# Kernel tuning notes

Measured on AMD Instinct MI355X. Metric: run time of the kernel, lower is better.

The kernel has to match this reference:

```python
import jax, jax.numpy as jnp
import numpy as np
from jax import lax

# pywt db4 filters (8 taps)
_DEC_LO = np.array([-0.010597401784997278, 0.032883011666982945, 0.030841381835986965,
                    -0.18703481171888114, -0.02798376941698385, 0.6308807679295904,
                    0.7148465705525415, 0.23037781330885523])
_DEC_HI = np.array([-0.23037781330885523, 0.7148465705525415, -0.6308807679295904,
                    -0.02798376941698385, 0.18703481171888114, 0.030841381835986965,
                    -0.032883011666982945, -0.010597401784997278])
_REC_LO = _DEC_LO[::-1].copy()
_REC_HI = _DEC_HI[::-1].copy()
_L = 8  # filter length
LEVELS = 4


def _dwt_level(x):
    # x: (M, n) -> (cA, cD) each (M, (n+_L-1)//2), pywt 'symmetric' mode
    xe = jnp.pad(x, ((0, 0), (_L - 1, _L - 1)), mode='symmetric')[:, 1:]
    ker = jnp.stack([_DEC_LO[::-1], _DEC_HI[::-1]]).astype(x.dtype)[:, None, :]  # (2,1,L)
    y = lax.conv_general_dilated(xe[:, None, :], ker, (2,), 'VALID')  # (M,2,m)
    return y[:, 0], y[:, 1]


def _idwt_level(ca, cd, out_len):
    # inverse DWT, cropped to out_len (matches length of next-finer approximation)
    inp = jnp.stack([ca, cd], axis=1)  # (M,2,m)
    ker = jnp.stack([_REC_LO[::-1], _REC_HI[::-1]]).astype(ca.dtype)[None]  # (1,2,L)
    y = lax.conv_general_dilated(inp, ker, (1,), [(_L - 1, _L - 1)], lhs_dilation=(2,))
    return y[:, 0, _L - 2:_L - 2 + out_len]


def setup_inputs() -> dict:
    key = jax.random.key(0)
    k1, k2, k3, k4 = jax.random.split(key, 4)
    B, N, C = 32, 8192, 64
    m = N
    for _ in range(LEVELS):
        m = (m + _L - 1) // 2  # 518
    scale = 1.0 / (C * C)
    return {
        'x': jax.random.normal(k1, (B, N, C), jnp.float32),
        'w1': scale * jax.random.uniform(k2, (C, C, m), jnp.float32),
        'w2': scale * jax.random.uniform(k3, (C, C, m), jnp.float32),
        'dense_kernel': jax.random.normal(k4, (C, C), jnp.float32) / jnp.sqrt(C).astype(jnp.float32),
        'dense_bias': jnp.zeros((C,), jnp.float32),
    }


def reference(x, w1, w2, dense_kernel, dense_bias):
    B, N, C = x.shape
    xc = jnp.transpose(x, (0, 2, 1)).reshape(B * C, N)  # per-(batch,channel) signals
    # analysis: multi-level DWT
    lens, details = [], []
    a = xc
    for _ in range(LEVELS):
        lens.append(a.shape[1])
        a, d = _dwt_level(a)
        details.append(d)
    m = a.shape[1]
    # channel mixing on coarsest approximation and coarsest detail (WNO kernel)
    a = jnp.einsum('bim,iom->bom', a.reshape(B, C, m), w1).reshape(B * C, m)
    details[-1] = jnp.einsum('bim,iom->bom', details[-1].reshape(B, C, m), w2).reshape(B * C, m)
    # synthesis: multi-level IDWT
    for j in range(LEVELS - 1, -1, -1):
        a = _idwt_level(a, details[j], lens[j])
    y = jnp.transpose(a.reshape(B, C, N), (0, 2, 1))
    shortcut = x @ dense_kernel + dense_bias  # Dense 1x1 shortcut
    out = y + shortcut
    return out * jnp.tanh(jax.nn.softplus(out))  # mish
```

## Files before the change

### kernel.cpp

```cpp
#include <hip/hip_runtime.h>
#include <hip/hip_bf16.h>
#include <stdint.h>

typedef __attribute__((ext_vector_type(8))) short short8;
typedef __attribute__((ext_vector_type(4))) float floatx4;

__device__ __constant__ float c_DL[8] = {
    -0.010597401784997278f, 0.032883011666982945f, 0.030841381835986965f,
    -0.18703481171888114f, -0.02798376941698385f, 0.6308807679295904f,
    0.7148465705525415f, 0.23037781330885523f};
__device__ __constant__ float c_DH[8] = {
    -0.23037781330885523f, 0.7148465705525415f, -0.6308807679295904f,
    -0.02798376941698385f, 0.18703481171888114f, 0.030841381835986965f,
    -0.032883011666982945f, -0.010597401784997278f};
__device__ __constant__ float c_RL[8] = {
    0.23037781330885523f, 0.7148465705525415f, 0.6308807679295904f,
    -0.02798376941698385f, -0.18703481171888114f, 0.030841381835986965f,
    0.032883011666982945f, -0.010597401784997278f};
__device__ __constant__ float c_RH[8] = {
    -0.010597401784997278f, -0.032883011666982945f, 0.030841381835986965f,
    0.18703481171888114f, -0.02798376941698385f, -0.6308807679295904f,
    0.7148465705525415f, -0.23037781330885523f};

__device__ __forceinline__ float bflo(uint32_t u) { return __uint_as_float(u << 16); }
__device__ __forceinline__ float bfhi(uint32_t u) { return __uint_as_float(u & 0xffff0000u); }
__device__ __forceinline__ float bfu(unsigned short u) { return __uint_as_float(((uint32_t)u) << 16); }
__device__ __forceinline__ short f2bs(float f) {
  __hip_bfloat16 h = __float2bfloat16(f);
  return *reinterpret_cast<short*>(&h);
}

__device__ __forceinline__ int reflect_idx(int t, int n) {
  if (t < 0) t = -1 - t;
  if (t >= n) t = 2 * n - 1 - t;
  return t;
}

#define S1R 4100
#define S2R 2056

__global__ __launch_bounds__(256) void k_wT(const float* __restrict__ w1,
                                            const float* __restrict__ w2,
                                            float* __restrict__ wt1,
                                            float* __restrict__ wt2) {
  const float* w = blockIdx.z ? w2 : w1;
  float* wt = blockIdx.z ? wt2 : wt1;
  const int io0 = blockIdx.x * 64;
  const int p0 = blockIdx.y * 64;
  const int pw = min(64, 518 - p0);
  const int tid = threadIdx.x;
  __shared__ float ts[64 * 65];
  for (int idx = tid; idx < 64 * 64; idx += 256) {
    int row = idx >> 6, col = idx & 63;
    if (col < pw) ts[row * 65 + col] = w[(size_t)(io0 + row) * 518 + p0 + col];
  }
  __syncthreads();
  for (int idx = tid; idx < 64 * 64; idx += 256) {
    int pl = idx >> 6, io = idx & 63;
    if (pl < pw) wt[(size_t)(p0 + pl) * 4096 + io0 + io] = ts[io * 65 + pl];
  }
}

#define NT1 134
#define XTS 138
__global__ __launch_bounds__(256) void k_dwt_first(const float* __restrict__ x,
                                                   __hip_bfloat16* __restrict__ outa,
                                                   __hip_bfloat16* __restrict__ outd) {
  const int b = blockIdx.y;
  const int k0 = blockIdx.x * 64;
  const int tid = threadIdx.x;
  __shared__ float xs[64 * XTS];

  const float4* x4 = (const float4*)x;
  for (int idx = tid; idx < NT1 * 16; idx += 256) {
    int nl = idx >> 4, cq = idx & 15;
    int t = 2 * k0 - 6 + nl;
    int n = reflect_idx(t, 8192);
    float4 v = x4[((size_t)b * 8192 + n) * 16 + cq];
    xs[(4 * cq + 0) * XTS + nl] = v.x;
    xs[(4 * cq + 1) * XTS + nl] = v.y;
    xs[(4 * cq + 2) * XTS + nl] = v.z;
    xs[(4 * cq + 3) * XTS + nl] = v.w;
  }
  __syncthreads();

  const int kk = tid & 63;
  const int k = k0 + kk;
  if (k >= 4099) return;
  for (int c = (tid >> 6); c < 64; c += 4) {
    const float2* p = (const float2*)&xs[c * XTS + 2 * kk];
    float2 p0 = p[0], p1 = p[1], p2 = p[2], p3 = p[3];
    float lo = c_DL[0] * p3.y + c_DL[1] * p3.x + c_DL[2] * p2.y + c_DL[3] * p2.x +
               c_DL[4] * p1.y + c_DL[5] * p1.x + c_DL[6] * p0.y + c_DL[7] * p0.x;
    float hi = c_DH[0] * p3.y + c_DH[1] * p3.x + c_DH[2] * p2.y + c_DH[3] * p2.x +
               c_DH[4] * p1.y + c_DH[5] * p1.x + c_DH[6] * p0.y + c_DH[7] * p0.x;
    size_t s = (size_t)b * 64 + c;
    outa[s * S1R + k] = __float2bfloat16(lo);
    outd[s * S1R + k] = __float2bfloat16(hi);
  }
}

__global__ __launch_bounds__(256) void k_ana234(const __hip_bfloat16* __restrict__ a1,
                                                __hip_bfloat16* __restrict__ d2o,
                                                float* __restrict__ d3o,
                                                float* __restrict__ a4o,
                                                float* __restrict__ d4o) {
  const int bid = blockIdx.x;
  const int s = (bid & 7) * 256 + (bid >> 3);
  const int i_ch = s >> 5;
  const int bb = s & 31;
  const int r = bb * 64 + i_ch;
  const int tid = threadIdx.x;
  __shared__ float s1[4100];
  __shared__ float s2[2054];
  __shared__ float s3[1032];

  const uint2* row2 = (const uint2*)(a1 + (size_t)r * S1R);
  for (int i = tid; i < 1025; i += 256) {
    uint2 u = row2[i];
    int e = 4 * i;
    s1[e] = bflo(u.x); s1[e + 1] = bfhi(u.x);
    s1[e + 2] = bflo(u.y); s1[e + 3] = bfhi(u.y);
  }
  __syncthreads();

  for (int k = tid; k < 2053; k += 256) {
    float lo = 0.f, hi = 0.f;
    if (k >= 3 && k <= 2048) {
      const float2* p = (const float2*)&s1[2 * k - 6];
      float2 v0 = p[0], v1 = p[1], v2 = p[2], v3 = p[3];
      lo = c_RL[0]*v0.x + c_RL[1]*v0.y + c_RL[2]*v1.x + c_RL[3]*v1.y +
           c_RL[4]*v2.x + c_RL[5]*v2.y + c_RL[6]*v3.x + c_RL[7]*v3.y;
      hi = c_RH[0]*v0.x + c_RH[1]*v0.y + c_RH[2]*v1.x + c_RH[3]*v1.y +
           c_RH[4]*v2.x + c_RH[5]*v2.y + c_RH[6]*v3.x + c_RH[7]*v3.y;
    } else {
#pragma unroll
      for (int j = 0; j < 8; ++j) {
        float v = s1[reflect_idx(2 * k + 1 - j, 4099)];
        lo += c_DL[j] * v; hi += c_DH[j] * v;
      }
    }
    d2o[(size_t)r * S2R + k] = __float2bfloat16(hi);
    s2[k] = lo;
  }
  __syncthreads();

  for (int k = tid; k < 1030; k += 256) {
    float lo = 0.f, hi = 0.f;
    if (k >= 3 && k <= 1025) {
      const float2* p = (const float2*)&s2[2 * k - 6];
      float2 v0 = p[0], v1 = p[1], v2 = p[2], v3 = p[3];
      lo = c_RL[0]*v0.x + c_RL[1]*v0.y + c_RL[2]*v1.x + c_RL[3]*v1.y +
           c_RL[4]*v2.x + c_RL[5]*v2.y + c_RL[6]*v3.x + c_RL[7]*v3.y;
      hi = c_RH[0]*v0.x + c_RH[1]*v0.y + c_RH[2]*v1.x + c_RH[3]*v1.y +
           c_RH[4]*v2.x + c_RH[5]*v2.y + c_RH[6]*v3.x + c_RH[7]*v3.y;
    } else {
#pragma unroll
      for (int j = 0; j < 8; ++j) {
        float v = s2[reflect_idx(2 * k + 1 - j, 2053)];
        lo += c_DL[j] * v; hi += c_DH[j] * v;
      }
    }
    d3o[(size_t)r * 1030 + k] = hi;
    s3[k] = lo;
  }
  __syncthreads();

  for (int k = tid; k < 518; k += 256) {
    float lo = 0.f, hi = 0.f;
    if (k >= 3 && k <= 514) {
      const float2* p = (const float2*)&s3[2 * k - 6];
      float2 v0 = p[0], v1 = p[1], v2 = p[2], v3 = p[3];
      lo = c_RL[0]*v0.x + c_RL[1]*v0.y + c_RL[2]*v1.x + c_RL[3]*v1.y +
           c_RL[4]*v2.x + c_RL[5]*v2.y + c_RL[6]*v3.x + c_RL[7]*v3.y;
      hi = c_RH[0]*v0.x + c_RH[1]*v0.y + c_RH[2]*v1.x + c_RH[3]*v1.y +
           c_RH[4]*v2.x + c_RH[5]*v2.y + c_RH[6]*v3.x + c_RH[7]*v3.y;
    } else {
#pragma unroll
      for (int j = 0; j < 8; ++j) {
        float v = s3[reflect_idx(2 * k + 1 - j, 1030)];
        lo += c_DL[j] * v; hi += c_DH[j] * v;
      }
    }
    a4o[(size_t)k * 2048 + s] = lo;
    d4o[(size_t)k * 2048 + s] = hi;
  }
}

__global__ __launch_bounds__(256) void k_mix_pc(const float* __restrict__ wt1,
                                                const float* __restrict__ wt2,
                                                const float* __restrict__ a4t,
                                                const float* __restrict__ d4t,
                                                float* __restrict__ am,
                                                float* __restrict__ dm) {
  const int bx = blockIdx.x;
  const int xcd = bx & 7;
  const int j = bx >> 3;
  const int p = (xcd < 6) ? (xcd * 65 + j) : (390 + (xcd - 6) * 64 + j);

  const float* w = blockIdx.y ? wt2 : wt1;
  const float* act = blockIdx.y ? d4t : a4t;
  float* outp = blockIdx.y ? dm : am;

  __shared__ float ws[4096];
  __shared__ float as_[2048];
  const int tid = threadIdx.x;

  const float4* wg = (const float4*)(w + (size_t)p * 4096);
  const float4* ag = (const float4*)(act + (size_t)p * 2048);
  float4* ws4 = (float4*)ws;
  float4* as4 = (float4*)as_;
  for (int t = tid; t < 1024; t += 256) ws4[t] = wg[t];
  for (int t = tid; t < 512; t += 256) as4[t] = ag[t];
  __syncthreads();

  const int o0 = (tid & 15) * 4;
  const int bq = tid >> 4;
  floatx4 acc0 = {0.f, 0.f, 0.f, 0.f}, acc1 = {0.f, 0.f, 0.f, 0.f};

#pragma unroll 8
  for (int i = 0; i < 64; ++i) {
    floatx4 wv = *(const floatx4*)&ws[i * 64 + o0];
    float a0 = as_[i * 32 + bq];
    float a1 = as_[i * 32 + bq + 16];
#pragma unroll
    for (int q = 0; q < 4; ++q) {
      acc0[q] += a0 * wv[q];
      acc1[q] += a1 * wv[q];
    }
  }

#pragma unroll
  for (int q = 0; q < 4; ++q) {
    outp[(size_t)(bq * 64 + o0 + q) * 518 + p] = acc0[q];
    outp[(size_t)((bq + 16) * 64 + o0 + q) * 518 + p] = acc1[q];
  }
}

#define RAS 68
__global__ __launch_bounds__(256) void k_epilogue(const float* __restrict__ a4m,
                                                  const float* __restrict__ d4m,
                                                  const float* __restrict__ d3,
                                                  const __hip_bfloat16* __restrict__ d2,
                                                  const __hip_bfloat16* __restrict__ dd1,
                                                  const float* __restrict__ x,
                                                  const float* __restrict__ dk,
                                                  const float* __restrict__ bias,
                                                  float* __restrict__ out) {
  const int b = blockIdx.y;
  const int bx = blockIdx.x;
  const int n0 = bx * 64;
  const int u0 = n0 >> 1;
  const int tid = threadIdx.x;
  const int lane = tid & 63;
  const int w = tid >> 6;

  __shared__ __hip_bfloat16 Ktf[4096];
  __shared__ float rds[36 * RAS];
  __shared__ float ras[36 * RAS];
  __shared__ float scr[6045];
  float* sa4 = scr;
  float* sd4 = scr + 650;
  float* sd3 = scr + 1300;
  float* sd2 = scr + 2210;
  float* r3s = scr + 3770;
  float* r2s = scr + 4680;

  {
    int o = tid & 63;
    int ot = o >> 4, m16o = o & 15;
    for (int it = 0; it < 2; ++it) {
      int slot = (tid >> 6) + 4 * it;
      int ks = slot >> 2, hi = slot & 3;
      int c0 = ks * 32 + hi * 8;
      short8 f;
#pragma unroll
      for (int kq2 = 0; kq2 < 8; ++kq2)
        f[kq2] = f2bs(dk[(size_t)(c0 + kq2) * 64 + o]);
      *(short8*)&Ktf[((ot * 2 + ks) * 64 + hi * 16 + m16o) * 8] = f;
    }
  }
  {
    const int o = tid & 63;
    const int part = tid >> 6;
    const size_t r = (size_t)b * 64 + o;
    if (part == 0) {
      const float2* pa = (const float2*)(a4m + r * 518 + bx * 4);
      const float2* pd = (const float2*)(d4m + r * 518 + bx * 4);
#pragma unroll
      for (int q = 0; q < 5; ++q) {
        float2 va = pa[q], vd = pd[q];
        sa4[(2 * q + 0) * 65 + o] = va.x; sa4[(2 * q + 1) * 65 + o] = va.y;
        sd4[(2 * q + 0) * 65 + o] = vd.x; sd4[(2 * q + 1) * 65 + o] = vd.y;
      }
    } else if (part == 1) {
      const float2* p3 = (const float2*)(d3 + r * 1030 + bx * 8);
#pragma unroll
      for (int q = 0; q < 7; ++q) {
        float2 v = p3[q];
        sd3[(2 * q + 0) * 65 + o] = v.x; sd3[(2 * q + 1) * 65 + o] = v.y;
      }
    } else if (part == 2) {
      const ushort4* p24 = (const ushort4*)(d2 + r * S2R + bx * 16);
#pragma unroll
      for (int q = 0; q < 6; ++q) {
        ushort4 v = p24[q];
        sd2[(4 * q + 0) * 65 + o] = bfu(v.x); sd2[(4 * q + 1) * 65 + o] = bfu(v.y);
        sd2[(4 * q + 2) * 65 + o] = bfu(v.z); sd2[(4 * q + 3) * 65 + o] = bfu(v.w);
      }
    } else {
      const ushort4* pd1 = (const ushort4*)(dd1 + r * S1R + u0);
#pragma unroll
      for (int q = 0; q < 9; ++q) {
        ushort4 v = pd1[q];
        int i0 = 4 * q;
        rds[(i0 + 0) * RAS + o] = bfu(v.x); rds[(i0 + 1) * RAS + o] = bfu(v.y);
        rds[(i0 + 2) * RAS + o] = bfu(v.z); rds[(i0 + 3) * RAS + o] = bfu(v.w);
      }
    }
  }
  __syncthreads();

  for (int it = tid; it < 14 * 64; it += 256) {
    int o = it & 63, wc = it >> 6;
    int base = wc >> 1, par = wc & 1;
    float acc = 0.f;
#pragma unroll
    for (int t = 0; t < 4; ++t) {
      int i = base + 3 - t;
      float fl = par ? c_RL[2 * t + 1] : c_RL[2 * t];
      float fh = par ? c_RH[2 * t + 1] : c_RH[2 * t];
      acc += fl * sa4[i * 65 + o] + fh * sd4[i * 65 + o];
    }
    r3s[wc * 65 + o] = acc;
  }
  __syncthreads();
  for (int it = tid; it < 21 * 64; it += 256) {
    int o = it & 63, vc = it >> 6;
    int base = vc >> 1, par = vc & 1;
    float acc = 0.f;
#pragma unroll
    for (int t = 0; t < 4; ++t) {
      int i = base + 3 - t;
      float fl = par ? c_RL[2 * t + 1] : c_RL[2 * t];
      float fh = par ? c_RH[2 * t + 1] : c_RH[2 * t];
      acc += fl * r3s[i * 65 + o] + fh * sd3[i * 65 + o];
    }
    r2s[vc * 65 + o] = acc;
  }
  __syncthreads();
  for (int it = tid; it < 35 * 64; it += 256) {
    int o = it & 63, uc = it >> 6;
    int base = uc >> 1, par = uc & 1;
    float acc = 0.f;
#pragma unroll
    for (int t = 0; t < 4; ++t) {
      int i = base + 3 - t;
      float fl = par ? c_RL[2 * t + 1] : c_RL[2 * t];
      float fh = par ? c_RH[2 * t + 1] : c_RH[2 * t];
      acc += fl * r2s[i * 65 + o] + fh * sd2[i * 65 + o];
    }
    ras[uc * RAS + o] = acc;
  }
  __syncthreads();

  const int m16 = lane & 15;
  const int kq = (lane >> 4) * 8;
  const int nrow = w * 16 + m16;
  const float* xrow = x + ((size_t)b * 8192 + n0 + nrow) * 64;

  floatx4 acc[4];
#pragma unroll
  for (int ot = 0; ot < 4; ++ot) acc[ot] = (floatx4){0.f, 0.f, 0.f, 0.f};

#pragma unroll
  for (int ks = 0; ks < 2; ++ks) {
    float4 xa = *(const float4*)(xrow + ks * 32 + kq);
    float4 xb = *(const float4*)(xrow + ks * 32 + kq + 4);
    short8 af;
    af[0] = f2bs(xa.x); af[1] = f2bs(xa.y); af[2] = f2bs(xa.z); af[3] = f2bs(xa.w);
    af[4] = f2bs(xb.x); af[5] = f2bs(xb.y); af[6] = f2bs(xb.z); af[7] = f2bs(xb.w);
#pragma unroll
    for (int ot = 0; ot < 4; ++ot) {
      short8 bf = *(const short8*)&Ktf[((ot * 2 + ks) * 64 + lane) * 8];
      acc[ot] = __builtin_amdgcn_mfma_f32_16x16x32_bf16(af, bf, acc[ot], 0, 0, 0);
    }
  }

  const int rbase = (lane >> 4) * 4;
#pragma unroll
  for (int ot = 0; ot < 4; ++ot) {
    int o_loc = ot * 16 + m16;
    float bo = bias[o_loc];
#pragma unroll
    for (int rg = 0; rg < 4; ++rg) {
      int n_loc = w * 16 + rbase + rg;
      int ul = n_loc >> 1, par = n_loc & 1;
      float wv = 0.f;
#pragma unroll
      for (int t = 0; t < 4; ++t) {
        int i = ul + 3 - t;
        float fl = par ? c_RL[2 * t + 1] : c_RL[2 * t];
        float fh = par ? c_RH[2 * t + 1] : c_RH[2 * t];
        wv += fl * ras[i * RAS + o_loc] + fh * rds[i * RAS + o_loc];
      }
      float v = acc[ot][rg] + wv + bo;
      float e = __expf(fminf(v, 15.f));
      float num = e * (e + 2.f);
      float mm = (v > 15.f) ? v : v * (num / (num + 2.f));
      __builtin_nontemporal_store(mm, &out[((size_t)b * 8192 + n0 + n_loc) * 64 + o_loc]);
    }
  }
}

extern "C" void kernel_launch(void* const* d_in, const int* in_sizes, int n_in,
                              void* d_out, int out_size, void* d_ws, size_t ws_size,
                              hipStream_t stream) {
  const float* x    = (const float*)d_in[0];
  const float* w1   = (const float*)d_in[1];
  const float* w2   = (const float*)d_in[2];
  const float* dk   = (const float*)d_in[3];
  const float* bias = (const float*)d_in[4];
  float* out = (float*)d_out;

  const size_t R = 2048;

  float* wf = (float*)d_ws;
  float* d3f = wf; wf += R * 1030;
  float* a4t = wf; wf += R * 518;
  float* d4t = wf; wf += R * 518;
  float* a4m = wf; wf += R * 518;
  float* d4m = wf; wf += R * 518;
  float* wt1 = wf; wf += (size_t)518 * 4096;
  float* wt2 = wf; wf += (size_t)518 * 4096;
  __hip_bfloat16* wb = (__hip_bfloat16*)wf;
  __hip_bfloat16* a1b = wb; wb += R * S1R;
  __hip_bfloat16* d1b = wb; wb += R * S1R;
  __hip_bfloat16* d2b = wb; wb += R * S2R;

  k_wT<<<dim3(64, 9, 2), 256, 0, stream>>>(w1, w2, wt1, wt2);
  k_dwt_first<<<dim3(65, 32), 256, 0, stream>>>(x, a1b, d1b);
  k_ana234<<<dim3(2048), 256, 0, stream>>>(a1b, d2b, d3f, a4t, d4t);
  k_mix_pc<<<dim3(518, 2), 256, 0, stream>>>(wt1, wt2, a4t, d4t, a4m, d4m);
  k_epilogue<<<dim3(128, 32), 256, 0, stream>>>(a4m, d4m, d3f, d2b, d1b, x, dk, bias, out);
}
```

Baseline: 267.6 us.

## Store detail coefficients position-major so epilogue loads coalesce across channels

Detail coefficients at levels 1–4 and the mixed coarse outputs move to a transposed layout (position-major, 2048 signals contiguous). Level-1 details are transposed through LDS inside the first DWT kernel. Levels 2 and 3 go through two new transpose kernels, and the mixing kernel now writes vectorised float4 rows. The goal is coalesced loads in the epilogue instead of strided per-row vector reads, at the cost of two extra launches, an extra pass over d2/d3, and reuse of the a1 buffer as d2t.

```diff
diff --git a/kernel.cpp b/kernel.cpp
--- a/kernel.cpp
+++ b/kernel.cpp
@@ -25,6 +25,10 @@
 __device__ __forceinline__ float bflo(uint32_t u) { return __uint_as_float(u << 16); }
 __device__ __forceinline__ float bfhi(uint32_t u) { return __uint_as_float(u & 0xffff0000u); }
 __device__ __forceinline__ float bfu(unsigned short u) { return __uint_as_float(((uint32_t)u) << 16); }
+__device__ __forceinline__ float ldf(const float* p, size_t i) { return p[i]; }
+__device__ __forceinline__ float ldf(const __hip_bfloat16* p, size_t i) { return __bfloat162float(p[i]); }
+__device__ __forceinline__ void stf(float* p, size_t i, float v) { p[i] = v; }
+__device__ __forceinline__ void stf(__hip_bfloat16* p, size_t i, float v) { p[i] = __float2bfloat16(v); }
 __device__ __forceinline__ short f2bs(float f) {
   __hip_bfloat16 h = __float2bfloat16(f);
   return *reinterpret_cast<short*>(&h);
@@ -65,11 +69,12 @@
 #define XTS 138
 __global__ __launch_bounds__(256) void k_dwt_first(const float* __restrict__ x,
                                                    __hip_bfloat16* __restrict__ outa,
-                                                   __hip_bfloat16* __restrict__ outd) {
+                                                   __hip_bfloat16* __restrict__ outdt) {
   const int b = blockIdx.y;
   const int k0 = blockIdx.x * 64;
   const int tid = threadIdx.x;
   __shared__ float xs[64 * XTS];
+  __shared__ __hip_bfloat16 lds_d[64 * 65];
 
   const float4* x4 = (const float4*)x;
   for (int idx = tid; idx < NT1 * 16; idx += 256) {
@@ -86,17 +91,24 @@
 
   const int kk = tid & 63;
   const int k = k0 + kk;
-  if (k >= 4099) return;
+  const bool act = (k < 4099);
   for (int c = (tid >> 6); c < 64; c += 4) {
-    const float2* p = (const float2*)&xs[c * XTS + 2 * kk];
-    float2 p0 = p[0], p1 = p[1], p2 = p[2], p3 = p[3];
-    float lo = c_DL[0] * p3.y + c_DL[1] * p3.x + c_DL[2] * p2.y + c_DL[3] * p2.x +
-               c_DL[4] * p1.y + c_DL[5] * p1.x + c_DL[6] * p0.y + c_DL[7] * p0.x;
-    float hi = c_DH[0] * p3.y + c_DH[1] * p3.x + c_DH[2] * p2.y + c_DH[3] * p2.x +
-               c_DH[4] * p1.y + c_DH[5] * p1.x + c_DH[6] * p0.y + c_DH[7] * p0.x;
-    size_t s = (size_t)b * 64 + c;
-    outa[s * S1R + k] = __float2bfloat16(lo);
-    outd[s * S1R + k] = __float2bfloat16(hi);
+    if (act) {
+      const float2* p = (const float2*)&xs[c * XTS + 2 * kk];
+      float2 p0 = p[0], p1 = p[1], p2 = p[2], p3 = p[3];
+      float lo = c_DL[0] * p3.y + c_DL[1] * p3.x + c_DL[2] * p2.y + c_DL[3] * p2.x +
+                 c_DL[4] * p1.y + c_DL[5] * p1.x + c_DL[6] * p0.y + c_DL[7] * p0.x;
+      float hi = c_DH[0] * p3.y + c_DH[1] * p3.x + c_DH[2] * p2.y + c_DH[3] * p2.x +
+                 c_DH[4] * p1.y + c_DH[5] * p1.x + c_DH[6] * p0.y + c_DH[7] * p0.x;
+      outa[((size_t)b * 64 + c) * S1R + k] = __float2bfloat16(lo);
+      lds_d[kk * 65 + c] = __float2bfloat16(hi);
+    }
+  }
+  __syncthreads();
+  for (int idx = tid; idx < 4096; idx += 256) {
+    int k_loc = idx >> 6, c = idx & 63;
+    if (k0 + k_loc < 4099)
+      outdt[(size_t)(k0 + k_loc) * 2048 + b * 64 + c] = lds_d[k_loc * 65 + c];
   }
 }
 
@@ -187,12 +199,30 @@
   }
 }
 
+template <typename T>
+__global__ __launch_bounds__(256) void k_t23(const T* __restrict__ src, T* __restrict__ dst,
+                                             int srcStride, int nk) {
+  const int k0 = blockIdx.x * 64;
+  const int r0 = blockIdx.y * 64;
+  const int tid = threadIdx.x;
+  __shared__ float ts[64 * 65];
+  for (int idx = tid; idx < 4096; idx += 256) {
+    int rl = idx >> 6, kl = idx & 63;
+    if (k0 + kl < nk) ts[rl * 65 + kl] = ldf(src, (size_t)(r0 + rl) * srcStride + k0 + kl);
+  }
+  __syncthreads();
+  for (int idx = tid; idx < 4096; idx += 256) {
+    int kl = idx >> 6, rl = idx & 63;
+    if (k0 + kl < nk) stf(dst, (size_t)(k0 + kl) * 2048 + r0 + rl, ts[rl * 65 + kl]);
+  }
+}
+
 __global__ __launch_bounds__(256) void k_mix_pc(const float* __restrict__ wt1,
                                                 const float* __restrict__ wt2,
                                                 const float* __restrict__ a4t,
                                                 const float* __restrict__ d4t,
-                                                float* __restrict__ am,
-                                                float* __restrict__ dm) {
+                                                float* __restrict__ amt,
+                                                float* __restrict__ dmt) {
   const int bx = blockIdx.x;
   const int xcd = bx & 7;
   const int j = bx >> 3;
@@ -200,7 +230,7 @@
 
   const float* w = blockIdx.y ? wt2 : wt1;
   const float* act = blockIdx.y ? d4t : a4t;
-  float* outp = blockIdx.y ? dm : am;
+  float* outp = blockIdx.y ? dmt : amt;
 
   __shared__ float ws[4096];
   __shared__ float as_[2048];
@@ -230,19 +260,16 @@
     }
   }
 
-#pragma unroll
-  for (int q = 0; q < 4; ++q) {
-    outp[(size_t)(bq * 64 + o0 + q) * 518 + p] = acc0[q];
-    outp[(size_t)((bq + 16) * 64 + o0 + q) * 518 + p] = acc1[q];
-  }
+  *(floatx4*)&outp[(size_t)p * 2048 + bq * 64 + o0] = acc0;
+  *(floatx4*)&outp[(size_t)p * 2048 + (bq + 16) * 64 + o0] = acc1;
 }
 
 #define RAS 68
-__global__ __launch_bounds__(256) void k_epilogue(const float* __restrict__ a4m,
-                                                  const float* __restrict__ d4m,
-                                                  const float* __restrict__ d3,
-                                                  const __hip_bfloat16* __restrict__ d2,
-                                                  const __hip_bfloat16* __restrict__ dd1,
+__global__ __launch_bounds__(256) void k_epilogue(const float* __restrict__ a4mt,
+                                                  const float* __restrict__ d4mt,
+                                                  const float* __restrict__ d3t,
+                                                  const __hip_bfloat16* __restrict__ d2t,
+                                                  const __hip_bfloat16* __restrict__ d1t,
                                                   const float* __restrict__ x,
                                                   const float* __restrict__ dk,
                                                   const float* __restrict__ bias,
@@ -281,42 +308,29 @@
     }
   }
   {
-    const int o = tid & 63;
-    const int part = tid >> 6;
-    const size_t r = (size_t)b * 64 + o;
-    if (part == 0) {
-      const float2* pa = (const float2*)(a4m + r * 518 + bx * 4);
-      const float2* pd = (const float2*)(d4m + r * 518 + bx * 4);
-#pragma unroll
-      for (int q = 0; q < 5; ++q) {
-        float2 va = pa[q], vd = pd[q];
-        sa4[(2 * q + 0) * 65 + o] = va.x; sa4[(2 * q + 1) * 65 + o] = va.y;
-        sd4[(2 * q + 0) * 65 + o] = vd.x; sd4[(2 * q + 1) * 65 + o] = vd.y;
+    const int o = lane;
+    const int rbase = b * 64 + o;
+    if (w == 0) {
+#pragma unroll
+      for (int j2 = 0; j2 < 10; ++j2) {
+        sa4[j2 * 65 + o] = a4mt[(size_t)(bx * 4 + j2) * 2048 + rbase];
+        sd4[j2 * 65 + o] = d4mt[(size_t)(bx * 4 + j2) * 2048 + rbase];
       }
-    } else if (part == 1) {
-      const float2* p3 = (const float2*)(d3 + r * 1030 + bx * 8);
-#pragma unroll
-      for (int q = 0; q < 7; ++q) {
-        float2 v = p3[q];
-        sd3[(2 * q + 0) * 65 + o] = v.x; sd3[(2 * q + 1) * 65 + o] = v.y;
-      }
-    } else if (part == 2) {
-      const ushort4* p24 = (const ushort4*)(d2 + r * S2R + bx * 16);
-#pragma unroll
-      for (int q = 0; q < 6; ++q) {
-        ushort4 v = p24[q];
-        sd2[(4 * q + 0) * 65 + o] = bfu(v.x); sd2[(4 * q + 1) * 65 + o] = bfu(v.y);
-        sd2[(4 * q + 2) * 65 + o] = bfu(v.z); sd2[(4 * q + 3) * 65 + o] = bfu(v.w);
-      }
+    } else if (w == 1) {
+#pragma unroll
+      for (int j2 = 0; j2 < 14; ++j2)
+        sd3[j2 * 65 + o] = d3t[(size_t)(bx * 8 + j2) * 2048 + rbase];
+#pragma unroll
+      for (int j2 = 25; j2 < 35; ++j2)
+        rds[j2 * RAS + o] = __bfloat162float(d1t[(size_t)(u0 + j2) * 2048 + rbase]);
+    } else if (w == 2) {
+#pragma unroll
+      for (int j2 = 0; j2 < 21; ++j2)
+        sd2[j2 * 65 + o] = __bfloat162float(d2t[(size_t)(bx * 16 + j2) * 2048 + rbase]);
     } else {
-      const ushort4* pd1 = (const ushort4*)(dd1 + r * S1R + u0);
-#pragma unroll
-      for (int q = 0; q < 9; ++q) {
-        ushort4 v = pd1[q];
-        int i0 = 4 * q;
-        rds[(i0 + 0) * RAS + o] = bfu(v.x); rds[(i0 + 1) * RAS + o] = bfu(v.y);
-        rds[(i0 + 2) * RAS + o] = bfu(v.z); rds[(i0 + 3) * RAS + o] = bfu(v.w);
-      }
+#pragma unroll
+      for (int j2 = 0; j2 < 25; ++j2)
+        rds[j2 * RAS + o] = __bfloat162float(d1t[(size_t)(u0 + j2) * 2048 + rbase]);
     }
   }
   __syncthreads();
@@ -387,14 +401,14 @@
     }
   }
 
-  const int rbase = (lane >> 4) * 4;
+  const int rbase2 = (lane >> 4) * 4;
 #pragma unroll
   for (int ot = 0; ot < 4; ++ot) {
     int o_loc = ot * 16 + m16;
     float bo = bias[o_loc];
 #pragma unroll
     for (int rg = 0; rg < 4; ++rg) {
-      int n_loc = w * 16 + rbase + rg;
+      int n_loc = w * 16 + rbase2 + rg;
       int ul = n_loc >> 1, par = n_loc & 1;
       float wv = 0.f;
 #pragma unroll
@@ -426,21 +440,25 @@
   const size_t R = 2048;
 
   float* wf = (float*)d_ws;
-  float* d3f = wf; wf += R * 1030;
-  float* a4t = wf; wf += R * 518;
-  float* d4t = wf; wf += R * 518;
-  float* a4m = wf; wf += R * 518;
-  float* d4m = wf; wf += R * 518;
-  float* wt1 = wf; wf += (size_t)518 * 4096;
-  float* wt2 = wf; wf += (size_t)518 * 4096;
+  float* d3f  = wf; wf += R * 1030;
+  float* d3t  = wf; wf += R * 1030;
+  float* a4t  = wf; wf += R * 518;
+  float* d4t  = wf; wf += R * 518;
+  float* a4mt = wf; wf += R * 518;
+  float* d4mt = wf; wf += R * 518;
+  float* wt1  = wf; wf += (size_t)518 * 4096;
+  float* wt2  = wf; wf += (size_t)518 * 4096;
   __hip_bfloat16* wb = (__hip_bfloat16*)wf;
   __hip_bfloat16* a1b = wb; wb += R * S1R;
-  __hip_bfloat16* d1b = wb; wb += R * S1R;
+  __hip_bfloat16* d1t = wb; wb += R * S1R;
   __hip_bfloat16* d2b = wb; wb += R * S2R;
+  __hip_bfloat16* d2t = a1b;
 
   k_wT<<<dim3(64, 9, 2), 256, 0, stream>>>(w1, w2, wt1, wt2);
-  k_dwt_first<<<dim3(65, 32), 256, 0, stream>>>(x, a1b, d1b);
+  k_dwt_first<<<dim3(65, 32), 256, 0, stream>>>(x, a1b, d1t);
   k_ana234<<<dim3(2048), 256, 0, stream>>>(a1b, d2b, d3f, a4t, d4t);
-  k_mix_pc<<<dim3(518, 2), 256, 0, stream>>>(wt1, wt2, a4t, d4t, a4m, d4m);
-  k_epilogue<<<dim3(128, 32), 256, 0, stream>>>(a4m, d4m, d3f, d2b, d1b, x, dk, bias, out);
-}
+  k_mix_pc<<<dim3(518, 2), 256, 0, stream>>>(wt1, wt2, a4t, d4t, a4mt, d4mt);
+  k_t23<__hip_bfloat16><<<dim3(33, 32), 256, 0, stream>>>(d2b, d2t, S2R, 2053);
+  k_t23<float><<<dim3(17, 32), 256, 0, stream>>>(d3f, d3t, 1030, 1030);
+  k_epilogue<<<dim3(128, 32), 256, 0, stream>>>(a4mt, d4mt, d3t, d2t, d1t, x, dk, bias, out);
+}
```

After: 266.8 us. Within noise of the previous version (-0.3%).
